# Kernel optimization log

Hardware: AMD Instinct MI355X
Metric: run time of the kernel (lower is better)

Reference implementation:

```python
import jax, jax.numpy as jnp
import numpy as np
from jax import lax


def setup_inputs() -> dict:
    key = jax.random.key(0)
    k1, k2, k3 = jax.random.split(key, 3)
    B, L, T = 1024, 512, 64
    logits = jax.random.normal(k1, (B, L, T), dtype=jnp.float32)
    tags = jax.random.randint(k2, (B, L), 0, T, dtype=jnp.int64)
    mask = jnp.ones((B, L), dtype=jnp.int32)
    trans_m = jax.random.normal(k3, (T, T), dtype=jnp.float32)
    return {"logits": logits, "tags": tags, "mask": mask, "trans_m": trans_m}


def _normalizer(logits_t, mask_t, trans):
    # logits_t: [L, B, T], mask_t: [L, B] float, trans: [T, T]
    alpha0 = logits_t[0]  # [B, T]

    def step(alpha, xs):
        emit, m = xs  # emit [B, T], m [B]
        # alpha[b, i] + trans[i, j] + emit[b, j] -> logsumexp over i
        tmp = alpha[:, :, None] + emit[:, None, :] + trans[None, :, :]  # [B, T, T]
        new_alpha = jax.nn.logsumexp(tmp, axis=1)  # [B, T]
        alpha = jnp.where(m[:, None] > 0, new_alpha, alpha)
        return alpha, None

    alpha, _ = lax.scan(step, alpha0, (logits_t[1:], mask_t[1:]))
    return jax.nn.logsumexp(alpha, axis=1)  # [B]


def _gold_score(logits_t, tags_t, mask_t, trans):
    # logits_t: [L, B, T], tags_t: [L, B] int, mask_t: [L, B] float
    # transition score between consecutive gold tags, masked where next pos is pad
    trans_score = trans[tags_t[:-1], tags_t[1:]] * mask_t[1:]  # [L-1, B]
    # emission score at gold tags, masked at pad positions
    emit = jnp.take_along_axis(logits_t, tags_t[:, :, None], axis=2)[:, :, 0] * mask_t  # [L, B]
    score = (trans_score + emit[:-1]).sum(axis=0) + emit[-1] * mask_t[-1]  # [B]
    return score


def reference(logits, tags, mask, trans_m):
    # forward: feats [B, L, T] -> transpose to [L, B, T]; loss = logZ - gold_score
    logits_t = jnp.transpose(logits, (1, 0, 2)).astype(jnp.float32)  # [L, B, T]
    tags_t = jnp.transpose(tags, (1, 0))  # [L, B]
    mask_t = jnp.transpose(mask, (1, 0)).astype(logits.dtype)  # [L, B]
    all_path = _normalizer(logits_t, mask_t, trans_m)
    gold = _gold_score(logits_t, tags_t, mask_t, trans_m)
    return all_path - gold  # [B] per-sample negative log-likelihood
```

## Files before the change

### kernel.cpp

```cpp
#include <hip/hip_runtime.h>
#include <math.h>


#define TDIM 64
typedef _Float16 h16;
typedef _Float16 v2h __attribute__((ext_vector_type(2)));

union H8 { float4 f4; v2h h[4]; };

#if defined(__has_builtin)
#if __has_builtin(__builtin_amdgcn_fdot2)
#define HAVE_FDOT2 1
#endif
#endif

__device__ __forceinline__ float dot2acc(v2h a, v2h b, float c) {
#ifdef HAVE_FDOT2
    return __builtin_amdgcn_fdot2(a, b, c, false);
#else
    return c + (float)a[0] * (float)b[0] + (float)a[1] * (float)b[1];
#endif
}

__device__ __forceinline__ float renorm(float v, int& kacc) {
    int rf = __builtin_amdgcn_readfirstlane(__float_as_int(v));
    int kk = ((rf >> 23) & 0xff) - 127 + 10;
    kacc += kk;
    return v * __uint_as_float((unsigned)(127 - kk) << 23);
}

__device__ __forceinline__ float step_dot(const h16* myQ, const v2h* epk) {
    const H8* pv = (const H8*)myQ;
    H8 f[8];
    #pragma unroll
    for (int i = 0; i < 8; ++i) f[i] = pv[i];
    float acc[8];
    #pragma unroll
    for (int i = 0; i < 8; ++i) {
        float a = dot2acc(f[i].h[0], epk[4 * i + 0], 0.f);
        a = dot2acc(f[i].h[1], epk[4 * i + 1], a);
        a = dot2acc(f[i].h[2], epk[4 * i + 2], a);
        a = dot2acc(f[i].h[3], epk[4 * i + 3], a);
        acc[i] = a;
    }
    float s01 = acc[0] + acc[1], s23 = acc[2] + acc[3];
    float s45 = acc[4] + acc[5], s67 = acc[6] + acc[7];
    return ((s01 + s23) + (s45 + s67));
}

__global__ __launch_bounds__(128, 1) void crf_fb_kernel(
    const float* __restrict__ logits,
    const int*   __restrict__ tags,
    const int*   __restrict__ mask,
    const float* __restrict__ trans,
    float* __restrict__ out,
    int L)
{
    const int tid = threadIdx.x;
    const int w   = tid >> 6;
    const int j   = tid & 63;
    const int b   = blockIdx.x;
    const int H   = L >> 1;

    __shared__ __align__(16) h16   Qs[2][TDIM];
    __shared__ __align__(16) int   smask[512];
    __shared__ __align__(16) float comb[2][TDIM];
    __shared__ float gpart[2];
    __shared__ float bpart[2];
    __shared__ int   kpart[2];

    const float* lb = logits + (size_t)b * L * TDIM;
    const int*   tb = tags + (size_t)b * L;
    const int*   mb = mask + (size_t)b * L;

    ((int4*)smask)[tid] = ((const int4*)mb)[tid];
    if (tid == 0) smask[0] = 0;
    __syncthreads();

    float g = 0.f;
    for (int t = w * H + j; t < (w + 1) * H; t += 64) {
        int   tag = tb[t];
        float mk  = (float)mb[t];
        float em  = lb[(size_t)t * TDIM + tag] * mk;
        float tr  = (t > 0) ? trans[tb[t - 1] * TDIM + tag] * mk : 0.f;
        g += em + tr;
    }
    #pragma unroll
    for (int o = 32; o >= 1; o >>= 1) g += __shfl_xor(g, o);

    v2h epk[32];
    #pragma unroll
    for (int p = 0; p < 32; ++p) {
        float a, c;
        if (w == 0) { a = __expf(trans[(2 * p) * TDIM + j]);
                      c = __expf(trans[(2 * p + 1) * TDIM + j]); }
        else        { a = __expf(trans[j * TDIM + 2 * p]);
                      c = __expf(trans[j * TDIM + 2 * p + 1]); }
        v2h t2 = {(h16)a, (h16)c};
        epk[p] = t2;
    }

    int kacc = 0;
    float base, q;
    h16* myQ = Qs[w];

    if (w == 0) {
        float a0 = lb[j];
        base = __int_as_float(__builtin_amdgcn_readfirstlane(__float_as_int(a0)));
        q = renorm(__expf(a0 - base), kacc);
        myQ[j] = (h16)q;

        float R[8], X[8];
        #pragma unroll
        for (int u = 0; u < 8; ++u) R[u] = lb[(size_t)u * TDIM + j];

        const int NB = H >> 3;
        for (int kb = 0; kb < NB; ++kb) {
            #pragma unroll
            for (int u = 0; u < 8; ++u) X[u] = __expf(R[u]);
            const int kn = (kb + 1 < NB) ? kb + 1 : kb;
            #pragma unroll
            for (int u = 0; u < 8; ++u)
                R[u] = lb[(size_t)(8 * kn + u) * TDIM + j];
            int4 mc0 = ((const int4*)smask)[kb * 2];
            int4 mc1 = ((const int4*)smask)[kb * 2 + 1];
            const int mks[8] = {mc0.x, mc0.y, mc0.z, mc0.w,
                                mc1.x, mc1.y, mc1.z, mc1.w};
            #pragma unroll
            for (int u = 0; u < 8; ++u) {
                __builtin_amdgcn_wave_barrier();
                float s = step_dot(myQ, epk);
                float q1 = s * X[u];
                q1 = (mks[u] > 0) ? q1 : q;
                q = renorm(q1, kacc);
                myQ[j] = (h16)q;
                __builtin_amdgcn_wave_barrier();
            }
        }
    } else {
        base = 0.f;
        q = 1.f;

        float R[8], X[8];
        #pragma unroll
        for (int u = 0; u < 8; ++u)
            R[u] = lb[(size_t)(L - 1 - u) * TDIM + j];

        const int NB = H >> 3;
        for (int kb = 0; kb < NB; ++kb) {
            #pragma unroll
            for (int u = 0; u < 8; ++u) X[u] = __expf(R[u]);
            const int kn = (kb + 1 < NB) ? kb + 1 : kb;
            #pragma unroll
            for (int u = 0; u < 8; ++u)
                R[u] = lb[(size_t)(L - 1 - 8 * kn - u) * TDIM + j];
            int mks[8];
            #pragma unroll
            for (int u = 0; u < 8; ++u) mks[u] = smask[L - 1 - 8 * kb - u];
            #pragma unroll
            for (int u = 0; u < 8; ++u) {
                float uv = q * X[u];
                myQ[j] = (h16)uv;
                __builtin_amdgcn_wave_barrier();
                float s = step_dot(myQ, epk);
                float z1 = (mks[u] > 0) ? s : q;
                q = renorm(z1, kacc);
                __builtin_amdgcn_wave_barrier();
            }
        }
    }

    comb[w][j] = q;
    if (j == 0) { gpart[w] = g; bpart[w] = base; kpart[w] = kacc; }
    __syncthreads();

    if (tid < 64) {
        float prod = comb[0][j] * comb[1][j];
        #pragma unroll
        for (int o = 32; o >= 1; o >>= 1) prod += __shfl_xor(prod, o);
        if (j == 0) {
            float logZ = bpart[0] + bpart[1]
                       + (float)(kpart[0] + kpart[1]) * 0.6931471805599453f
                       + __logf(prod);
            out[b] = logZ - (gpart[0] + gpart[1]);
        }
    }
}

extern "C" void kernel_launch(void* const* d_in, const int* in_sizes, int n_in,
                              void* d_out, int out_size, void* d_ws, size_t ws_size,
                              hipStream_t stream) {
    const float* logits = (const float*)d_in[0];
    const int*   tags   = (const int*)d_in[1];
    const int*   mask   = (const int*)d_in[2];
    const float* trans  = (const float*)d_in[3];
    float* out = (float*)d_out;

    const int B = out_size;
    const int L = in_sizes[1] / B;

    crf_fb_kernel<<<B, 128, 0, stream>>>(logits, tags, mask, trans, out, L);
}
```

Before: 247.7 us.

## Batch 16 sequences per wave and run forward-backward recurrence on MFMA

Replaces the per-sequence dot2 recurrence, which used shared-memory exchange each step, with a 16x16x32 f16 MFMA formulation. Each wave now advances 16 batch rows at once, keeping the state in registers, and renormalizes scale per batch column. Gold-score computation moves to two separate waves, and a fast path skips mask selects when every mask entry is set. It also launches far fewer blocks (B/16) of 256 threads, which may leave compute units idle and changes how latency is hidden.

```diff
diff --git a/kernel.cpp b/kernel.cpp
--- a/kernel.cpp
+++ b/kernel.cpp
@@ -3,52 +3,154 @@
 
 
 #define TDIM 64
-typedef _Float16 h16;
-typedef _Float16 v2h __attribute__((ext_vector_type(2)));
-
-union H8 { float4 f4; v2h h[4]; };
-
-#if defined(__has_builtin)
-#if __has_builtin(__builtin_amdgcn_fdot2)
-#define HAVE_FDOT2 1
-#endif
-#endif
-
-__device__ __forceinline__ float dot2acc(v2h a, v2h b, float c) {
-#ifdef HAVE_FDOT2
-    return __builtin_amdgcn_fdot2(a, b, c, false);
-#else
-    return c + (float)a[0] * (float)b[0] + (float)a[1] * (float)b[1];
-#endif
-}
-
-__device__ __forceinline__ float renorm(float v, int& kacc) {
-    int rf = __builtin_amdgcn_readfirstlane(__float_as_int(v));
-    int kk = ((rf >> 23) & 0xff) - 127 + 10;
-    kacc += kk;
-    return v * __uint_as_float((unsigned)(127 - kk) << 23);
-}
-
-__device__ __forceinline__ float step_dot(const h16* myQ, const v2h* epk) {
-    const H8* pv = (const H8*)myQ;
-    H8 f[8];
-    #pragma unroll
-    for (int i = 0; i < 8; ++i) f[i] = pv[i];
-    float acc[8];
-    #pragma unroll
-    for (int i = 0; i < 8; ++i) {
-        float a = dot2acc(f[i].h[0], epk[4 * i + 0], 0.f);
-        a = dot2acc(f[i].h[1], epk[4 * i + 1], a);
-        a = dot2acc(f[i].h[2], epk[4 * i + 2], a);
-        a = dot2acc(f[i].h[3], epk[4 * i + 3], a);
-        acc[i] = a;
-    }
-    float s01 = acc[0] + acc[1], s23 = acc[2] + acc[3];
-    float s45 = acc[4] + acc[5], s67 = acc[6] + acc[7];
-    return ((s01 + s23) + (s45 + s67));
-}
-
-__global__ __launch_bounds__(128, 1) void crf_fb_kernel(
+typedef _Float16 f16;
+typedef _Float16 f16x2 __attribute__((ext_vector_type(2)));
+typedef _Float16 f16x8 __attribute__((ext_vector_type(8)));
+typedef float    f32x4 __attribute__((ext_vector_type(4)));
+
+union B8 { f16x8 v; f16x2 p[4]; };
+
+#define MFMA16(A, B, C) __builtin_amdgcn_mfma_f32_16x16x32_f16((A), (B), (C), 0, 0, 0)
+
+__device__ __forceinline__ f16x2 pk2(float a, float b) {
+    f16x2 r; r[0] = (f16)a; r[1] = (f16)b; return r;
+}
+
+template <int DIR>
+__device__ __forceinline__ void run_chain(
+    const float* __restrict__ lp,
+    const int*   __restrict__ mrow,
+    const float* __restrict__ trans,
+    int L, int ml, int gl, bool masked,
+    float a[16], int& kacc)
+{
+    f16x8 Af[4][2];
+    #pragma unroll
+    for (int c = 0; c < 4; ++c) {
+        const int mlog = 32*(c>>1) + 8*(ml>>2) + 4*(c&1) + (ml&3);
+        #pragma unroll
+        for (int kc = 0; kc < 2; ++kc) {
+            B8 t;
+            #pragma unroll
+            for (int e = 0; e < 8; e += 2) {
+                const int k0 = 32*kc + 8*gl + e;
+                float x0, x1;
+                if (DIR == 0) { x0 = trans[k0*TDIM + mlog];  x1 = trans[(k0+1)*TDIM + mlog]; }
+                else          { x0 = trans[mlog*TDIM + k0];  x1 = trans[mlog*TDIM + k0 + 1]; }
+                t.p[e>>1] = pk2(__expf(x0), __expf(x1));
+            }
+            Af[c][kc] = t.v;
+        }
+    }
+
+    #pragma unroll
+    for (int i = 0; i < 16; ++i) a[i] = 1.f;
+    kacc = 0;
+
+    const int xo0 = 8*gl, xo1 = 8*gl + 4, xo2 = 8*gl + 32, xo3 = 8*gl + 36;
+
+    float4 Rf[4][4];
+    #pragma unroll
+    for (int u = 0; u < 4; ++u) {
+        const int t = (DIR == 0) ? u : (L - 1 - u);
+        const float* pt = lp + (size_t)t * TDIM;
+        Rf[u][0] = *(const float4*)(pt + xo0);
+        Rf[u][1] = *(const float4*)(pt + xo1);
+        Rf[u][2] = *(const float4*)(pt + xo2);
+        Rf[u][3] = *(const float4*)(pt + xo3);
+    }
+
+    float Xc[16];
+    #pragma unroll
+    for (int c = 0; c < 4; ++c) {
+        Xc[c*4+0] = __expf(Rf[0][c].x); Xc[c*4+1] = __expf(Rf[0][c].y);
+        Xc[c*4+2] = __expf(Rf[0][c].z); Xc[c*4+3] = __expf(Rf[0][c].w);
+    }
+
+    const int NS = L >> 1;
+    for (int kb = 0; kb < NS/4; ++kb) {
+        #pragma unroll
+        for (int u = 0; u < 4; ++u) {
+            const int st = 4*kb + u;
+            const int t  = (DIR == 0) ? st : (L - 1 - st);
+
+            float cand[16];
+            if (DIR == 0 && st == 0) {
+                #pragma unroll
+                for (int i = 0; i < 16; ++i) cand[i] = Xc[i];
+            } else {
+                float bsrc[16];
+                #pragma unroll
+                for (int i = 0; i < 16; ++i) bsrc[i] = (DIR == 0) ? a[i] : a[i]*Xc[i];
+                B8 b0, b1;
+                #pragma unroll
+                for (int h = 0; h < 4; ++h) {
+                    b0.p[h] = pk2(bsrc[2*h],     bsrc[2*h+1]);
+                    b1.p[h] = pk2(bsrc[8 + 2*h], bsrc[8 + 2*h+1]);
+                }
+                f32x4 D0 = {0.f,0.f,0.f,0.f}, D1 = {0.f,0.f,0.f,0.f};
+                f32x4 D2 = {0.f,0.f,0.f,0.f}, D3 = {0.f,0.f,0.f,0.f};
+                D0 = MFMA16(Af[0][0], b0.v, D0); D0 = MFMA16(Af[0][1], b1.v, D0);
+                D1 = MFMA16(Af[1][0], b0.v, D1); D1 = MFMA16(Af[1][1], b1.v, D1);
+                D2 = MFMA16(Af[2][0], b0.v, D2); D2 = MFMA16(Af[2][1], b1.v, D2);
+                D3 = MFMA16(Af[3][0], b0.v, D3); D3 = MFMA16(Af[3][1], b1.v, D3);
+                if (DIR == 0) {
+                    #pragma unroll
+                    for (int r = 0; r < 4; ++r) {
+                        cand[r]      = D0[r] * Xc[r];
+                        cand[4 + r]  = D1[r] * Xc[4 + r];
+                        cand[8 + r]  = D2[r] * Xc[8 + r];
+                        cand[12 + r] = D3[r] * Xc[12 + r];
+                    }
+                } else {
+                    #pragma unroll
+                    for (int r = 0; r < 4; ++r) {
+                        cand[r] = D0[r]; cand[4+r] = D1[r];
+                        cand[8+r] = D2[r]; cand[12+r] = D3[r];
+                    }
+                }
+                if (masked) {
+                    const int m = mrow[t];
+                    #pragma unroll
+                    for (int i = 0; i < 16; ++i) cand[i] = (m > 0) ? cand[i] : a[i];
+                }
+            }
+
+            {
+                int sn = st + 4; if (sn >= NS) sn = st;
+                const int tn = (DIR == 0) ? sn : (L - 1 - sn);
+                const float* pn = lp + (size_t)tn * TDIM;
+                Rf[u][0] = *(const float4*)(pn + xo0);
+                Rf[u][1] = *(const float4*)(pn + xo1);
+                Rf[u][2] = *(const float4*)(pn + xo2);
+                Rf[u][3] = *(const float4*)(pn + xo3);
+            }
+            float Xn[16];
+            {
+                const int un = (u + 1) & 3;
+                #pragma unroll
+                for (int c = 0; c < 4; ++c) {
+                    Xn[c*4+0] = __expf(Rf[un][c].x); Xn[c*4+1] = __expf(Rf[un][c].y);
+                    Xn[c*4+2] = __expf(Rf[un][c].z); Xn[c*4+3] = __expf(Rf[un][c].w);
+                }
+            }
+
+            {
+                const float ref = __shfl(cand[0], ml);
+                const int eb = (__float_as_int(ref) >> 23) & 255;
+                const int kk = eb - 117;
+                kacc += kk;
+                const float s = __int_as_float((unsigned)(244 - eb) << 23);
+                #pragma unroll
+                for (int i = 0; i < 16; ++i) a[i] = cand[i] * s;
+            }
+            #pragma unroll
+            for (int i = 0; i < 16; ++i) Xc[i] = Xn[i];
+        }
+    }
+}
+
+__global__ __launch_bounds__(256, 1) void crf_mfma_kernel(
     const float* __restrict__ logits,
     const int*   __restrict__ tags,
     const int*   __restrict__ mask,
@@ -58,131 +160,72 @@
 {
     const int tid = threadIdx.x;
     const int w   = tid >> 6;
-    const int j   = tid & 63;
-    const int b   = blockIdx.x;
-    const int H   = L >> 1;
-
-    __shared__ __align__(16) h16   Qs[2][TDIM];
-    __shared__ __align__(16) int   smask[512];
-    __shared__ __align__(16) float comb[2][TDIM];
-    __shared__ float gpart[2];
-    __shared__ float bpart[2];
-    __shared__ int   kpart[2];
-
-    const float* lb = logits + (size_t)b * L * TDIM;
-    const int*   tb = tags + (size_t)b * L;
-    const int*   mb = mask + (size_t)b * L;
-
-    ((int4*)smask)[tid] = ((const int4*)mb)[tid];
-    if (tid == 0) smask[0] = 0;
+    const int l   = tid & 63;
+    const int ml  = l & 15;
+    const int gl  = l >> 4;
+    const int bg  = blockIdx.x * 16;
+    const int bi  = bg + ml;
+
+    __shared__ __align__(16) float zfin[64][16];
+    __shared__ float gpart2[2][16];
+    __shared__ int   kbuf[16];
+
+    float a[16];
+    int   kacc = 0;
+
+    if (w >= 2) {
+        const int t0 = (w - 2) * (L >> 1);
+        const int*   tb  = tags + (size_t)bi * L;
+        const int*   mb  = mask + (size_t)bi * L;
+        const float* lbg = logits + (size_t)bi * L * TDIM;
+        float gs = 0.f;
+        #pragma unroll 4
+        for (int i = 0; i < (L >> 3); ++i) {
+            const int t  = t0 + gl + 4*i;
+            const int tg = tb[t];
+            const float mk = (float)mb[t];
+            const float em = lbg[(size_t)t * TDIM + tg];
+            const float tr = (t > 0) ? trans[tb[t-1] * TDIM + tg] : 0.f;
+            gs += mk * (em + tr);
+        }
+        gs += __shfl_xor(gs, 16);
+        gs += __shfl_xor(gs, 32);
+        if (l < 16) gpart2[w - 2][l] = gs;
+    } else {
+        const float* lp   = logits + (size_t)bi * L * TDIM;
+        const int*   mrow = mask + (size_t)bi * L;
+        const int t0 = (w == 0) ? 0 : (L >> 1);
+        bool ok = true;
+        {
+            const int4* m4 = (const int4*)(mrow + t0);
+            #pragma unroll 4
+            for (int i = 0; i < 16; ++i) {
+                const int4 v = m4[gl * 16 + i];
+                ok = ok && (v.x > 0) && (v.y > 0) && (v.z > 0) && (v.w > 0);
+            }
+        }
+        const bool masked = !__all(ok ? 1 : 0);
+        if (w == 0) run_chain<0>(lp, mrow, trans, L, ml, gl, masked, a, kacc);
+        else        run_chain<1>(lp, mrow, trans, L, ml, gl, masked, a, kacc);
+        if (w == 1) {
+            #pragma unroll
+            for (int i = 0; i < 16; ++i) zfin[l][i] = a[i];
+            if (l < 16) kbuf[l] = kacc;
+        }
+    }
+
     __syncthreads();
 
-    float g = 0.f;
-    for (int t = w * H + j; t < (w + 1) * H; t += 64) {
-        int   tag = tb[t];
-        float mk  = (float)mb[t];
-        float em  = lb[(size_t)t * TDIM + tag] * mk;
-        float tr  = (t > 0) ? trans[tb[t - 1] * TDIM + tag] * mk : 0.f;
-        g += em + tr;
-    }
-    #pragma unroll
-    for (int o = 32; o >= 1; o >>= 1) g += __shfl_xor(g, o);
-
-    v2h epk[32];
-    #pragma unroll
-    for (int p = 0; p < 32; ++p) {
-        float a, c;
-        if (w == 0) { a = __expf(trans[(2 * p) * TDIM + j]);
-                      c = __expf(trans[(2 * p + 1) * TDIM + j]); }
-        else        { a = __expf(trans[j * TDIM + 2 * p]);
-                      c = __expf(trans[j * TDIM + 2 * p + 1]); }
-        v2h t2 = {(h16)a, (h16)c};
-        epk[p] = t2;
-    }
-
-    int kacc = 0;
-    float base, q;
-    h16* myQ = Qs[w];
-
     if (w == 0) {
-        float a0 = lb[j];
-        base = __int_as_float(__builtin_amdgcn_readfirstlane(__float_as_int(a0)));
-        q = renorm(__expf(a0 - base), kacc);
-        myQ[j] = (h16)q;
-
-        float R[8], X[8];
+        float prod = 0.f;
         #pragma unroll
-        for (int u = 0; u < 8; ++u) R[u] = lb[(size_t)u * TDIM + j];
-
-        const int NB = H >> 3;
-        for (int kb = 0; kb < NB; ++kb) {
-            #pragma unroll
-            for (int u = 0; u < 8; ++u) X[u] = __expf(R[u]);
-            const int kn = (kb + 1 < NB) ? kb + 1 : kb;
-            #pragma unroll
-            for (int u = 0; u < 8; ++u)
-                R[u] = lb[(size_t)(8 * kn + u) * TDIM + j];
-            int4 mc0 = ((const int4*)smask)[kb * 2];
-            int4 mc1 = ((const int4*)smask)[kb * 2 + 1];
-            const int mks[8] = {mc0.x, mc0.y, mc0.z, mc0.w,
-                                mc1.x, mc1.y, mc1.z, mc1.w};
-            #pragma unroll
-            for (int u = 0; u < 8; ++u) {
-                __builtin_amdgcn_wave_barrier();
-                float s = step_dot(myQ, epk);
-                float q1 = s * X[u];
-                q1 = (mks[u] > 0) ? q1 : q;
-                q = renorm(q1, kacc);
-                myQ[j] = (h16)q;
-                __builtin_amdgcn_wave_barrier();
-            }
-        }
-    } else {
-        base = 0.f;
-        q = 1.f;
-
-        float R[8], X[8];
-        #pragma unroll
-        for (int u = 0; u < 8; ++u)
-            R[u] = lb[(size_t)(L - 1 - u) * TDIM + j];
-
-        const int NB = H >> 3;
-        for (int kb = 0; kb < NB; ++kb) {
-            #pragma unroll
-            for (int u = 0; u < 8; ++u) X[u] = __expf(R[u]);
-            const int kn = (kb + 1 < NB) ? kb + 1 : kb;
-            #pragma unroll
-            for (int u = 0; u < 8; ++u)
-                R[u] = lb[(size_t)(L - 1 - 8 * kn - u) * TDIM + j];
-            int mks[8];
-            #pragma unroll
-            for (int u = 0; u < 8; ++u) mks[u] = smask[L - 1 - 8 * kb - u];
-            #pragma unroll
-            for (int u = 0; u < 8; ++u) {
-                float uv = q * X[u];
-                myQ[j] = (h16)uv;
-                __builtin_amdgcn_wave_barrier();
-                float s = step_dot(myQ, epk);
-                float z1 = (mks[u] > 0) ? s : q;
-                q = renorm(z1, kacc);
-                __builtin_amdgcn_wave_barrier();
-            }
-        }
-    }
-
-    comb[w][j] = q;
-    if (j == 0) { gpart[w] = g; bpart[w] = base; kpart[w] = kacc; }
-    __syncthreads();
-
-    if (tid < 64) {
-        float prod = comb[0][j] * comb[1][j];
-        #pragma unroll
-        for (int o = 32; o >= 1; o >>= 1) prod += __shfl_xor(prod, o);
-        if (j == 0) {
-            float logZ = bpart[0] + bpart[1]
-                       + (float)(kpart[0] + kpart[1]) * 0.6931471805599453f
-                       + __logf(prod);
-            out[b] = logZ - (gpart[0] + gpart[1]);
+        for (int i = 0; i < 16; ++i) prod += a[i] * zfin[l][i];
+        prod += __shfl_xor(prod, 16);
+        prod += __shfl_xor(prod, 32);
+        if (l < 16) {
+            const float logZ = (float)(kacc + kbuf[l]) * 0.6931471805599453f
+                             + __logf(prod);
+            out[bg + l] = logZ - (gpart2[0][l] + gpart2[1][l]);
         }
     }
 }
@@ -199,5 +242,5 @@
     const int B = out_size;
     const int L = in_sizes[1] / B;
 
-    crf_fb_kernel<<<B, 128, 0, stream>>>(logits, tags, mask, trans, out, L);
-}
+    crf_mfma_kernel<<<B / 16, 256, 0, stream>>>(logits, tags, mask, trans, out, L);
+}
```

Measured after the change: 279.8 us. 12.9% more time.
